# Kernel optimization log

Measured on AMD Instinct MI355X. Metric: run time of the kernel, lower is better.

The kernel has to match this reference:

```python
import jax, jax.numpy as jnp
import numpy as np

PARENTS = [-1, 0, 0, 0, 1, 2, 3, 4, 5, 6, 7, 8, 9, 9, 9, 12, 13, 14, 16, 17, 18, 19, 20, 21]
K = 24          # num_joints (SMPL kinematic tree)
BONE = 12       # 3x3 rotation (9) + 3 rel offset
FEAT = 64       # local_feature_size
B = 65536       # batch
NIN = BONE + 1 + FEAT  # 77: bone_transform(13) concat parent feature(64)


def setup_inputs() -> dict:
    key = jax.random.key(0)
    ks = jax.random.split(key, 6)
    pose = jax.random.normal(ks[0], (B, K, 3, 3), jnp.float32)
    rel_joints = jax.random.normal(ks[1], (B, K, 3), jnp.float32)
    # proj_bone_prior: Linear(K*BONE -> FEAT)
    Wp = jax.random.normal(ks[2], (K * BONE, FEAT), jnp.float32) * 0.05
    bp = jnp.zeros((FEAT,), jnp.float32)
    # per-joint BoneMLP: Linear(NIN->NIN), ReLU, Linear(NIN->FEAT), ReLU (stacked over K)
    W1 = jax.random.normal(ks[3], (K, NIN, NIN), jnp.float32) * 0.05
    b1 = jnp.zeros((K, NIN), jnp.float32)
    W2 = jax.random.normal(ks[4], (K, NIN, FEAT), jnp.float32) * 0.05
    b2 = jnp.zeros((K, FEAT), jnp.float32)
    return {"pose": pose, "rel_joints": rel_joints, "Wp": Wp, "bp": bp,
            "W1": W1, "b1": b1, "W2": W2, "b2": b2}


def reference(pose, rel_joints, Wp, bp, W1, b1, W2, b2):
    Bn, Kn = rel_joints.shape[0], rel_joints.shape[1]
    bone_lengths = jnp.linalg.norm(rel_joints, axis=-1, keepdims=True)          # B,K,1
    bone_features = jnp.concatenate([pose.reshape(Bn, Kn, 9), rel_joints], -1)  # B,K,12
    root_bone_prior = bone_features.reshape(Bn, -1) @ Wp + bp                   # B,FEAT
    bone_transforms = jnp.concatenate([bone_features, bone_lengths], -1)        # B,K,13
    feats = [None] * Kn
    for i in range(Kn):  # fixed structural loop over kinematic tree (K=24)
        parent = PARENTS[i]
        pf = root_bone_prior if parent == -1 else feats[parent]
        x = jnp.concatenate([bone_transforms[:, i, :], pf], axis=-1)  # B,77
        h = jax.nn.relu(x @ W1[i] + b1[i])
        feats[i] = jax.nn.relu(h @ W2[i] + b2[i])
    return jnp.concatenate(feats, axis=-1)  # B, K*FEAT
```

## Files before the change

### kernel.cpp

```cpp
#include <hip/hip_runtime.h>
#include <hip/hip_bf16.h>
#include <math.h>

typedef __attribute__((ext_vector_type(8))) short short8;
typedef __attribute__((ext_vector_type(4))) short s4;
typedef __attribute__((ext_vector_type(4))) float f32x4;

#define NJ 24

#define F1_J   7680
#define F2_OFF (NJ*F1_J)
#define F2_J   6144
#define FP_OFF (F2_OFF + NJ*F2_J)
#define IMG_SHORTS (FP_OFF + 36*512)

#define MFMA(A,B,C) __builtin_amdgcn_mfma_f32_16x16x32_bf16((A),(B),(C),0,0,0)

__constant__ int ORD[24] = {0,1,4,7,10, 2,5,8,11, 3,6,9, 12,15, 13,16,18,20,22, 14,17,19,21,23};
__constant__ int PSL[24] = {2,0,1,1,1,  0,1,1,1,  0,0,0,  0,1,   0,1,1,1,1,    0,0,0,0,0};
__constant__ int SSL[24] = {0,1,1,1,-1, 1,1,1,-1, 0,0,0,  1,-1,  1,1,1,1,-1,   0,0,0,0,-1};

__device__ __forceinline__ short f2bf(float f) {
  union { float f; unsigned u; } v; v.f = f;
  unsigned r = v.u + 0x7FFFu + ((v.u >> 16) & 1u);
  return (short)(r >> 16);
}
__device__ __forceinline__ short sbf(float f) {
  __hip_bfloat16 h = __float2bfloat16(f);
  return *reinterpret_cast<short*>(&h);
}
__device__ __forceinline__ short8 pk8(f32x4 lo, f32x4 hi) {
  union { short8 s; unsigned u[4]; } r;
  asm("v_cvt_pk_bf16_f32 %0, %1, %2" : "=v"(r.u[0]) : "v"(lo[0]), "v"(lo[1]));
  asm("v_cvt_pk_bf16_f32 %0, %1, %2" : "=v"(r.u[1]) : "v"(lo[2]), "v"(lo[3]));
  asm("v_cvt_pk_bf16_f32 %0, %1, %2" : "=v"(r.u[2]) : "v"(hi[0]), "v"(hi[1]));
  asm("v_cvt_pk_bf16_f32 %0, %1, %2" : "=v"(r.u[3]) : "v"(hi[2]), "v"(hi[3]));
  return r.s;
}
__device__ __forceinline__ s4 pk4(f32x4 v) {
  union { s4 s; unsigned u[2]; } r;
  asm("v_cvt_pk_bf16_f32 %0, %1, %2" : "=v"(r.u[0]) : "v"(v[0]), "v"(v[1]));
  asm("v_cvt_pk_bf16_f32 %0, %1, %2" : "=v"(r.u[1]) : "v"(v[2]), "v"(v[3]));
  return r.s;
}
__device__ __forceinline__ f32x4 relu4(f32x4 v) {
  f32x4 r; r[0]=fmaxf(v[0],0.f); r[1]=fmaxf(v[1],0.f);
  r[2]=fmaxf(v[2],0.f); r[3]=fmaxf(v[3],0.f); return r;
}

__global__ __launch_bounds__(256) void prep_kernel(
    const float* __restrict__ W1, const float* __restrict__ W2,
    const float* __restrict__ Wp, const float* __restrict__ b1,
    const float* __restrict__ b2, short* __restrict__ img) {
  int t = blockIdx.x * 256 + threadIdx.x;
  if (t >= IMG_SHORTS) return;
  float v = 0.f;
  if (t < F2_OFF) {
    int i = t / F1_J, r = t % F1_J;
    int blk = r >> 9, q = r & 511;
    int ln = q >> 3, e = q & 7;
    int nt = blk / 3, s = blk - nt*3;
    int n  = nt*16 + (ln & 15);
    int kp = s*32 + (ln >> 4)*8 + e;
    if (kp == 13) {
      v = (n < 77) ? b1[i*77 + n] : (n == 77 ? 1.f : 0.f);
    } else if (n < 77) {
      if (kp < 13)                  v = W1[i*5929 + kp*77 + n];
      else if (kp >= 16 && kp < 80) v = W1[i*5929 + (kp-3)*77 + n];
    }
  } else if (t < FP_OFF) {
    int u = t - F2_OFF;
    int i = u / F2_J, r = u % F2_J;
    int blk = r >> 9, q = r & 511;
    int ln = q >> 3, e = q & 7;
    int nt = blk / 3, s = blk - nt*3;
    int n  = nt*16 + (ln & 15);
    int k  = s*32 + (ln >> 4)*8 + e;
    if (k < 77)       v = W2[i*4928 + k*64 + n];
    else if (k == 77) v = b2[i*64 + n];
  } else {
    int u = t - FP_OFF;
    int blk = u >> 9, q = u & 511;
    int ln = q >> 3, e = q & 7;
    int nt = blk / 9, s = blk - nt*9;
    int n  = nt*16 + (ln & 15);
    int kp = s*32 + (ln >> 4)*8 + e;
    int j, w;
    if (kp < 216) { j = kp / 9;       w = kp % 9; }
    else          { j = (kp-216) / 3; w = 9 + (kp-216) % 3; }
    v = Wp[(j*12 + w)*64 + n];
  }
  img[t] = f2bf(v);
}

#define ISSUE_W1(JN) do { \
  unsigned long long _b = img_u + (unsigned long long)(JN)*15360ull; \
  asm volatile( \
    "global_load_dwordx4 %0, %15, %16\n"  "global_load_dwordx4 %1, %15, %16 offset:1024\n" \
    "global_load_dwordx4 %2, %15, %16 offset:2048\n" "global_load_dwordx4 %3, %15, %16 offset:3072\n" \
    "global_load_dwordx4 %4, %15, %17\n"  "global_load_dwordx4 %5, %15, %17 offset:1024\n" \
    "global_load_dwordx4 %6, %15, %17 offset:2048\n" "global_load_dwordx4 %7, %15, %17 offset:3072\n" \
    "global_load_dwordx4 %8, %15, %18\n"  "global_load_dwordx4 %9, %15, %18 offset:1024\n" \
    "global_load_dwordx4 %10, %15, %18 offset:2048\n" "global_load_dwordx4 %11, %15, %18 offset:3072\n" \
    "global_load_dwordx4 %12, %15, %19\n" "global_load_dwordx4 %13, %15, %19 offset:1024\n" \
    "global_load_dwordx4 %14, %15, %19 offset:2048\n" \
    : "=&v"(fw1[0]),"=&v"(fw1[1]),"=&v"(fw1[2]),"=&v"(fw1[3]),"=&v"(fw1[4]), \
      "=&v"(fw1[5]),"=&v"(fw1[6]),"=&v"(fw1[7]),"=&v"(fw1[8]),"=&v"(fw1[9]), \
      "=&v"(fw1[10]),"=&v"(fw1[11]),"=&v"(fw1[12]),"=&v"(fw1[13]),"=&v"(fw1[14]) \
    : "v"(voff), "s"(_b), "s"(_b+4096ull), "s"(_b+8192ull), "s"(_b+12288ull) \
    : "memory"); \
} while(0)

#define ISSUE_BTW2(J) do { \
  unsigned long long _b = img_u + 368640ull + (unsigned long long)(J)*12288ull; \
  asm volatile( \
    "global_load_dword %0, %20, off\n" \
    "global_load_dword %1, %20, off offset:4\n" \
    "global_load_dword %2, %20, off offset:8\n" \
    "global_load_dword %3, %20, off offset:12\n" \
    "global_load_dword %4, %21, %22\n" \
    "global_load_dword %5, %21, %22 offset:4\n" \
    "global_load_dword %6, %21, %22 offset:8\n" \
    "global_load_dword %7, %21, %22 offset:12\n" \
    "global_load_dwordx4 %8, %23, %24\n"  "global_load_dwordx4 %9, %23, %24 offset:1024\n" \
    "global_load_dwordx4 %10, %23, %24 offset:2048\n" "global_load_dwordx4 %11, %23, %24 offset:3072\n" \
    "global_load_dwordx4 %12, %23, %25\n" "global_load_dwordx4 %13, %23, %25 offset:1024\n" \
    "global_load_dwordx4 %14, %23, %25 offset:2048\n" "global_load_dwordx4 %15, %23, %25 offset:3072\n" \
    "global_load_dwordx4 %16, %23, %26\n" "global_load_dwordx4 %17, %23, %26 offset:1024\n" \
    "global_load_dwordx4 %18, %23, %26 offset:2048\n" "global_load_dwordx4 %19, %23, %26 offset:3072\n" \
    : "=&v"(d0),"=&v"(d1),"=&v"(d2),"=&v"(d3),"=&v"(d4),"=&v"(d5),"=&v"(d6),"=&v"(d7), \
      "=&v"(fw2[0]),"=&v"(fw2[1]),"=&v"(fw2[2]),"=&v"(fw2[3]),"=&v"(fw2[4]),"=&v"(fw2[5]), \
      "=&v"(fw2[6]),"=&v"(fw2[7]),"=&v"(fw2[8]),"=&v"(fw2[9]),"=&v"(fw2[10]),"=&v"(fw2[11]) \
    : "v"(aA), "v"(vB), "s"(pose_u), "v"(voff), \
      "s"(_b), "s"(_b+4096ull), "s"(_b+8192ull) \
    : "memory"); \
} while(0)

#define WAITV(N) do { asm volatile("s_waitcnt vmcnt(" #N ")" ::: "memory"); \
                      __builtin_amdgcn_sched_barrier(0); } while(0)

__global__ __launch_bounds__(256, 2) void enc_kernel(
    const float* __restrict__ pose, const float* __restrict__ rel,
    const float* __restrict__ bp,  const short* __restrict__ img,
    float* __restrict__ out) {
  __shared__ __align__(16) short lds[4*10240];

  const int tid  = threadIdx.x;
  const int lane = tid & 63;
  const int wv   = tid >> 6;
  short* myl   = lds + wv*10240;
  short* featL = myl;
  short* hL    = myl + 6912;
  short* btL   = myl + 9472;

  const int cl  = lane & 15;
  const int g   = lane >> 4;
  const int rw0 = blockIdx.x*128 + wv*32;
  const short8 zz = {0,0,0,0,0,0,0,0};
  const unsigned long long img_u  = (unsigned long long)img;
  const unsigned long long pose_u = (unsigned long long)pose;
  const unsigned long long rel_u  = (unsigned long long)rel;
  const unsigned voff = (unsigned)lane << 4;
  const int btr = lane >> 1, btq = lane & 1;
  const unsigned btProw = (unsigned)((rw0 + btr)*864);
  const unsigned btRrow = (unsigned)((rw0 + btr)*288);

  short8 fw1[15], fw2[12];
  float d0, d1, d2, d3, d4, d5, d6, d7;

  {
    const float* pb = pose + (size_t)(rw0 + btr)*216;
    const float* rb = rel  + (size_t)(rw0 + btr)*72;
    short8 w;
    if (btq == 0) {
      w = pk8(*(const f32x4*)pb, *(const f32x4*)(pb + 4));
    } else {
      float r0 = rb[0], r1 = rb[1], r2 = rb[2];
      float nv = sqrtf(r0*r0 + r1*r1 + r2*r2);
      w[0]=sbf(pb[8]); w[1]=sbf(r0); w[2]=sbf(r1); w[3]=sbf(r2);
      w[4]=sbf(nv); w[5]=(short)0x3F80; w[6]=0; w[7]=0;
    }
    *(short8*)(btL + btr*24 + btq*8) = w;
  }
  f32x4 bpv[4];
#pragma unroll
  for (int nt = 0; nt < 4; ++nt) bpv[nt] = *(const f32x4*)(bp + nt*16 + g*4);

  f32x4 racc[2][4] = {};
  {
    const float* pr0 = pose + (size_t)(rw0 + cl)*216;
    const float* rr0 = rel  + (size_t)(rw0 + cl)*72;
    const float* pr1 = pose + (size_t)(rw0 + 16 + cl)*216;
    const float* rr1 = rel  + (size_t)(rw0 + 16 + cl)*72;
    const short8* fpg = (const short8*)(img + FP_OFF) + lane;
    short8 av0[9], av1[9];
#pragma unroll
    for (int s = 0; s < 9; ++s) {
      int k0 = s*32 + g*8;
      const float* s0 = (k0 < 216) ? (pr0 + k0) : (rr0 + (k0 - 216));
      const float* s1 = (k0 < 216) ? (pr1 + k0) : (rr1 + (k0 - 216));
      av0[s] = pk8(*(const f32x4*)s0, *(const f32x4*)(s0 + 4));
      av1[s] = pk8(*(const f32x4*)s1, *(const f32x4*)(s1 + 4));
    }
#pragma unroll
    for (int nt = 0; nt < 4; ++nt) {
      short8 fwp[9];
#pragma unroll
      for (int s = 0; s < 9; ++s) fwp[s] = fpg[(nt*9 + s)*64];
#pragma unroll
      for (int s = 0; s < 9; ++s) {
        racc[0][nt] = MFMA(fwp[s], av0[s], racc[0][nt]);
        racc[1][nt] = MFMA(fwp[s], av1[s], racc[1][nt]);
      }
    }
  }
#pragma unroll
  for (int nt = 0; nt < 4; ++nt) {
#pragma unroll
    for (int m = 0; m < 2; ++m) {
      f32x4 v = racc[m][nt];
      v[0]+=bpv[nt][0]; v[1]+=bpv[nt][1]; v[2]+=bpv[nt][2]; v[3]+=bpv[nt][3];
      *(s4*)(featL + 2*2304 + (m*16 + cl)*72 + nt*16 + g*4) = pk4(v);
    }
  }

  ISSUE_W1(0);

#pragma unroll 1
  for (int p = 0; p < NJ; ++p) {
    const int j  = ORD[p];
    const int ps = PSL[p];
    const int ss = SSL[p];
    const int jn = (p < NJ-1) ? ORD[p+1] : 0;

    const short* fb0 = featL + ps*2304 + cl*72;
    const short* fb1 = featL + ps*2304 + (16 + cl)*72;
    short8 a0[2], a1[2], a2[2];
    a0[0] = (g < 2) ? *(const short8*)(btL + cl*24 + g*8)
                    : *(const short8*)(fb0 + (g-2)*8);
    a0[1] = (g < 2) ? *(const short8*)(btL + (16+cl)*24 + g*8)
                    : *(const short8*)(fb1 + (g-2)*8);
    a1[0] = *(const short8*)(fb0 + 16 + g*8);
    a1[1] = *(const short8*)(fb1 + 16 + g*8);
    a2[0] = (g < 2) ? *(const short8*)(fb0 + 48 + g*8) : zz;
    a2[1] = (g < 2) ? *(const short8*)(fb1 + 48 + g*8) : zz;

    const unsigned long long aA =
        btq ? (rel_u  + btRrow + (unsigned)(jn ? jn*12 - 4 : 0))
            : (pose_u + btProw + (unsigned)(jn*36));
    const unsigned vB = btProw + (unsigned)(jn*36) + (btq ? 20u : 16u);
    ISSUE_BTW2(j);

    if (p == 0) { WAITV(20); } else { WAITV(28); }

#pragma unroll
    for (int nt = 0; nt < 5; ++nt) {
      f32x4 c0 = {0,0,0,0}, c1 = {0,0,0,0};
      c0 = MFMA(fw1[nt*3+0], a0[0], c0);  c1 = MFMA(fw1[nt*3+0], a0[1], c1);
      c0 = MFMA(fw1[nt*3+1], a1[0], c0);  c1 = MFMA(fw1[nt*3+1], a1[1], c1);
      c0 = MFMA(fw1[nt*3+2], a2[0], c0);  c1 = MFMA(fw1[nt*3+2], a2[1], c1);
      *(s4*)(hL + cl*80 + nt*16 + g*4)        = pk4(relu4(c0));
      *(s4*)(hL + (16 + cl)*80 + nt*16 + g*4) = pk4(relu4(c1));
    }
    short8 h0[2], h1[2], h2[2];
#pragma unroll
    for (int m = 0; m < 2; ++m) {
      const short* hb = hL + (m*16 + cl)*80;
      h0[m] = *(const short8*)(hb + g*8);
      h1[m] = *(const short8*)(hb + 32 + g*8);
      h2[m] = (g < 2) ? *(const short8*)(hb + 64 + g*8) : zz;
    }

    ISSUE_W1(jn);
    WAITV(15);

    {
      f32x4 lo = {d0, d1, d2, d3}, hi = {d4, d5, d6, d7};
      short8 wA = pk8(lo, hi);
      float r0 = jn ? d1 : d0;
      float r1 = jn ? d2 : d1;
      float r2 = jn ? d3 : d2;
      float nv = sqrtf(r0*r0 + r1*r1 + r2*r2);
      short8 wB;
      wB[0]=sbf(d7);   wB[1]=sbf(r0); wB[2]=sbf(r1); wB[3]=sbf(r2);
      wB[4]=sbf(nv); wB[5]=(short)0x3F80; wB[6]=0; wB[7]=0;
      short8 w = btq ? wB : wA;
      *(short8*)(btL + btr*24 + btq*8) = w;
    }

#pragma unroll
    for (int nt = 0; nt < 4; ++nt) {
      f32x4 c0 = {0,0,0,0}, c1 = {0,0,0,0};
      c0 = MFMA(fw2[nt*3+0], h0[0], c0);  c1 = MFMA(fw2[nt*3+0], h0[1], c1);
      c0 = MFMA(fw2[nt*3+1], h1[0], c0);  c1 = MFMA(fw2[nt*3+1], h1[1], c1);
      c0 = MFMA(fw2[nt*3+2], h2[0], c0);  c1 = MFMA(fw2[nt*3+2], h2[1], c1);
      f32x4 v0 = relu4(c0), v1 = relu4(c1);
      float* o0 = out + (size_t)(rw0 + cl)*1536      + (size_t)j*64 + nt*16 + g*4;
      float* o1 = out + (size_t)(rw0 + 16 + cl)*1536 + (size_t)j*64 + nt*16 + g*4;
      __builtin_nontemporal_store(v0, (f32x4*)o0);
      __builtin_nontemporal_store(v1, (f32x4*)o1);
      if (ss >= 0) {
        *(s4*)(featL + ss*2304 + cl*72 + nt*16 + g*4)        = pk4(v0);
        *(s4*)(featL + ss*2304 + (16 + cl)*72 + nt*16 + g*4) = pk4(v1);
      }
    }
  }
}

extern "C" void kernel_launch(void* const* d_in, const int* in_sizes, int n_in,
                              void* d_out, int out_size, void* d_ws, size_t ws_size,
                              hipStream_t stream) {
  const float* pose = (const float*)d_in[0];
  const float* rel  = (const float*)d_in[1];
  const float* Wp   = (const float*)d_in[2];
  const float* bp   = (const float*)d_in[3];
  const float* W1   = (const float*)d_in[4];
  const float* b1   = (const float*)d_in[5];
  const float* W2   = (const float*)d_in[6];
  const float* b2   = (const float*)d_in[7];
  float* outp = (float*)d_out;
  short* img  = (short*)d_ws;
  const int Bn = in_sizes[0] / 216;
  prep_kernel<<<(IMG_SHORTS + 255)/256, 256, 0, stream>>>(W1, W2, Wp, b1, b2, img);
  enc_kernel<<<Bn/128, 256, 0, stream>>>(pose, rel, bp, img, outp);
}
```

Measured before the change: 153.4 us.

## Double-buffer W1 fragments and prefetch weights two joints ahead

Splits the W1 register fragments into two alternating buffers so W1 for joint p+2 is loaded while joint p computes, and moves the W2/bone-transform loads to the end of each iteration so they prefetch one joint ahead. The loop is unrolled by two to alternate buffers, the wait counts are re-tuned, and the W2 loads are reordered ahead of the dword loads. The bone-transform LDS row stride also shrinks from 24 to 16. This lengthens the load-to-use distance to hide global latency, at the cost of 15 more short8 registers per thread, which may hurt occupancy or spill under launch_bounds(256,2).

```diff
diff --git a/kernel.cpp b/kernel.cpp
--- a/kernel.cpp
+++ b/kernel.cpp
@@ -93,7 +93,7 @@
   img[t] = f2bf(v);
 }
 
-#define ISSUE_W1(JN) do { \
+#define ISSUE_W1_INTO(ARR, JN) do { \
   unsigned long long _b = img_u + (unsigned long long)(JN)*15360ull; \
   asm volatile( \
     "global_load_dwordx4 %0, %15, %16\n"  "global_load_dwordx4 %1, %15, %16 offset:1024\n" \
@@ -104,9 +104,9 @@
     "global_load_dwordx4 %10, %15, %18 offset:2048\n" "global_load_dwordx4 %11, %15, %18 offset:3072\n" \
     "global_load_dwordx4 %12, %15, %19\n" "global_load_dwordx4 %13, %15, %19 offset:1024\n" \
     "global_load_dwordx4 %14, %15, %19 offset:2048\n" \
-    : "=&v"(fw1[0]),"=&v"(fw1[1]),"=&v"(fw1[2]),"=&v"(fw1[3]),"=&v"(fw1[4]), \
-      "=&v"(fw1[5]),"=&v"(fw1[6]),"=&v"(fw1[7]),"=&v"(fw1[8]),"=&v"(fw1[9]), \
-      "=&v"(fw1[10]),"=&v"(fw1[11]),"=&v"(fw1[12]),"=&v"(fw1[13]),"=&v"(fw1[14]) \
+    : "=&v"(ARR[0]),"=&v"(ARR[1]),"=&v"(ARR[2]),"=&v"(ARR[3]),"=&v"(ARR[4]), \
+      "=&v"(ARR[5]),"=&v"(ARR[6]),"=&v"(ARR[7]),"=&v"(ARR[8]),"=&v"(ARR[9]), \
+      "=&v"(ARR[10]),"=&v"(ARR[11]),"=&v"(ARR[12]),"=&v"(ARR[13]),"=&v"(ARR[14]) \
     : "v"(voff), "s"(_b), "s"(_b+4096ull), "s"(_b+8192ull), "s"(_b+12288ull) \
     : "memory"); \
 } while(0)
@@ -114,6 +114,12 @@
 #define ISSUE_BTW2(J) do { \
   unsigned long long _b = img_u + 368640ull + (unsigned long long)(J)*12288ull; \
   asm volatile( \
+    "global_load_dwordx4 %8, %23, %24\n"  "global_load_dwordx4 %9, %23, %24 offset:1024\n" \
+    "global_load_dwordx4 %10, %23, %24 offset:2048\n" "global_load_dwordx4 %11, %23, %24 offset:3072\n" \
+    "global_load_dwordx4 %12, %23, %25\n" "global_load_dwordx4 %13, %23, %25 offset:1024\n" \
+    "global_load_dwordx4 %14, %23, %25 offset:2048\n" "global_load_dwordx4 %15, %23, %25 offset:3072\n" \
+    "global_load_dwordx4 %16, %23, %26\n" "global_load_dwordx4 %17, %23, %26 offset:1024\n" \
+    "global_load_dwordx4 %18, %23, %26 offset:2048\n" "global_load_dwordx4 %19, %23, %26 offset:3072\n" \
     "global_load_dword %0, %20, off\n" \
     "global_load_dword %1, %20, off offset:4\n" \
     "global_load_dword %2, %20, off offset:8\n" \
@@ -122,12 +128,6 @@
     "global_load_dword %5, %21, %22 offset:4\n" \
     "global_load_dword %6, %21, %22 offset:8\n" \
     "global_load_dword %7, %21, %22 offset:12\n" \
-    "global_load_dwordx4 %8, %23, %24\n"  "global_load_dwordx4 %9, %23, %24 offset:1024\n" \
-    "global_load_dwordx4 %10, %23, %24 offset:2048\n" "global_load_dwordx4 %11, %23, %24 offset:3072\n" \
-    "global_load_dwordx4 %12, %23, %25\n" "global_load_dwordx4 %13, %23, %25 offset:1024\n" \
-    "global_load_dwordx4 %14, %23, %25 offset:2048\n" "global_load_dwordx4 %15, %23, %25 offset:3072\n" \
-    "global_load_dwordx4 %16, %23, %26\n" "global_load_dwordx4 %17, %23, %26 offset:1024\n" \
-    "global_load_dwordx4 %18, %23, %26 offset:2048\n" "global_load_dwordx4 %19, %23, %26 offset:3072\n" \
     : "=&v"(d0),"=&v"(d1),"=&v"(d2),"=&v"(d3),"=&v"(d4),"=&v"(d5),"=&v"(d6),"=&v"(d7), \
       "=&v"(fw2[0]),"=&v"(fw2[1]),"=&v"(fw2[2]),"=&v"(fw2[3]),"=&v"(fw2[4]),"=&v"(fw2[5]), \
       "=&v"(fw2[6]),"=&v"(fw2[7]),"=&v"(fw2[8]),"=&v"(fw2[9]),"=&v"(fw2[10]),"=&v"(fw2[11]) \
@@ -138,6 +138,91 @@
 
 #define WAITV(N) do { asm volatile("s_waitcnt vmcnt(" #N ")" ::: "memory"); \
                       __builtin_amdgcn_sched_barrier(0); } while(0)
+
+#define BODY(P, FW, CWAIT) do { \
+    const int j  = ORD[P]; \
+    const int ps = PSL[P]; \
+    const int ss = SSL[P]; \
+    const int jw2 = ((P)+1 < NJ) ? ORD[(P)+1] : 0; \
+    const int jd  = ((P)+1 < NJ) ? ORD[(P)+1] : 0; \
+    const int jb  = ((P)+2 < NJ) ? ORD[(P)+2] : 0; \
+    const int jw1 = ((P)+2 < NJ) ? ORD[(P)+2] : 0; \
+     \
+    const short* fb0 = featL + ps*2304 + cl*72; \
+    const short* fb1 = featL + ps*2304 + (16 + cl)*72; \
+    short8 a0[2], a1[2], a2[2]; \
+    a0[0] = (g < 2) ? *(const short8*)(btL + cl*16 + g*8) \
+                    : *(const short8*)(fb0 + (g-2)*8); \
+    a0[1] = (g < 2) ? *(const short8*)(btL + (16+cl)*16 + g*8) \
+                    : *(const short8*)(fb1 + (g-2)*8); \
+    a1[0] = *(const short8*)(fb0 + 16 + g*8); \
+    a1[1] = *(const short8*)(fb1 + 16 + g*8); \
+    a2[0] = (g < 2) ? *(const short8*)(fb0 + 48 + g*8) : zz; \
+    a2[1] = (g < 2) ? *(const short8*)(fb1 + 48 + g*8) : zz; \
+     \
+    WAITV(CWAIT); \
+     \
+    _Pragma("unroll") \
+    for (int nt = 0; nt < 5; ++nt) { \
+      f32x4 c0 = {0,0,0,0}, c1 = {0,0,0,0}; \
+      c0 = MFMA(FW[nt*3+0], a0[0], c0);  c1 = MFMA(FW[nt*3+0], a0[1], c1); \
+      c0 = MFMA(FW[nt*3+1], a1[0], c0);  c1 = MFMA(FW[nt*3+1], a1[1], c1); \
+      c0 = MFMA(FW[nt*3+2], a2[0], c0);  c1 = MFMA(FW[nt*3+2], a2[1], c1); \
+      *(s4*)(hL + cl*80 + nt*16 + g*4)        = pk4(relu4(c0)); \
+      *(s4*)(hL + (16 + cl)*80 + nt*16 + g*4) = pk4(relu4(c1)); \
+    } \
+     \
+    short8 h0[2], h1[2], h2[2]; \
+    _Pragma("unroll") \
+    for (int m = 0; m < 2; ++m) { \
+      const short* hb = hL + (m*16 + cl)*80; \
+      h0[m] = *(const short8*)(hb + g*8); \
+      h1[m] = *(const short8*)(hb + 32 + g*8); \
+      h2[m] = (g < 2) ? *(const short8*)(hb + 64 + g*8) : zz; \
+    } \
+     \
+    WAITV(15); \
+     \
+    { \
+      f32x4 lo = {d0, d1, d2, d3}, hi = {d4, d5, d6, d7}; \
+      short8 wA = pk8(lo, hi); \
+      float r0 = jd ? d1 : d0; \
+      float r1 = jd ? d2 : d1; \
+      float r2 = jd ? d3 : d2; \
+      float nv = sqrtf(r0*r0 + r1*r1 + r2*r2); \
+      short8 wB; \
+      wB[0]=sbf(d7);   wB[1]=sbf(r0); wB[2]=sbf(r1); wB[3]=sbf(r2); \
+      wB[4]=sbf(nv); wB[5]=(short)0x3F80; wB[6]=0; wB[7]=0; \
+      short8 w = btq ? wB : wA; \
+      *(short8*)(btL + btr*16 + btq*8) = w; \
+    } \
+     \
+    _Pragma("unroll") \
+    for (int nt = 0; nt < 4; ++nt) { \
+      f32x4 c0 = {0,0,0,0}, c1 = {0,0,0,0}; \
+      c0 = MFMA(fw2[nt*3+0], h0[0], c0);  c1 = MFMA(fw2[nt*3+0], h0[1], c1); \
+      c0 = MFMA(fw2[nt*3+1], h1[0], c0);  c1 = MFMA(fw2[nt*3+1], h1[1], c1); \
+      c0 = MFMA(fw2[nt*3+2], h2[0], c0);  c1 = MFMA(fw2[nt*3+2], h2[1], c1); \
+      f32x4 v0 = relu4(c0), v1 = relu4(c1); \
+      float* o0 = out + (size_t)(rw0 + cl)*1536      + (size_t)j*64 + nt*16 + g*4; \
+      float* o1 = out + (size_t)(rw0 + 16 + cl)*1536 + (size_t)j*64 + nt*16 + g*4; \
+      __builtin_nontemporal_store(v0, (f32x4*)o0); \
+      __builtin_nontemporal_store(v1, (f32x4*)o1); \
+      if (ss >= 0) { \
+        *(s4*)(featL + ss*2304 + cl*72 + nt*16 + g*4)        = pk4(v0); \
+        *(s4*)(featL + ss*2304 + (16 + cl)*72 + nt*16 + g*4) = pk4(v1); \
+      } \
+    } \
+     \
+    { \
+      const unsigned long long aA = \
+          btq ? (rel_u  + btRrow + (unsigned)(jb ? jb*12 - 4 : 0)) \
+              : (pose_u + btProw + (unsigned)(jb*36)); \
+      const unsigned vB = btProw + (unsigned)(jb*36) + (btq ? 20u : 16u); \
+      ISSUE_BTW2(jw2); \
+    } \
+    ISSUE_W1_INTO(FW, jw1); \
+  } while(0)
 
 __global__ __launch_bounds__(256, 2) void enc_kernel(
     const float* __restrict__ pose, const float* __restrict__ rel,
@@ -165,7 +250,7 @@
   const unsigned btProw = (unsigned)((rw0 + btr)*864);
   const unsigned btRrow = (unsigned)((rw0 + btr)*288);
 
-  short8 fw1[15], fw2[12];
+  short8 fw1a[15], fw1b[15], fw2[12];
   float d0, d1, d2, d3, d4, d5, d6, d7;
 
   {
@@ -180,7 +265,7 @@
       w[0]=sbf(pb[8]); w[1]=sbf(r0); w[2]=sbf(r1); w[3]=sbf(r2);
       w[4]=sbf(nv); w[5]=(short)0x3F80; w[6]=0; w[7]=0;
     }
-    *(short8*)(btL + btr*24 + btq*8) = w;
+    *(short8*)(btL + btr*16 + btq*8) = w;
   }
   f32x4 bpv[4];
 #pragma unroll
@@ -224,86 +309,24 @@
     }
   }
 
-  ISSUE_W1(0);
-
+  {
+    const int jb = ORD[1];
+    const unsigned long long aA =
+        btq ? (rel_u  + btRrow + (unsigned)(jb*12 - 4))
+            : (pose_u + btProw + (unsigned)(jb*36));
+    const unsigned vB = btProw + (unsigned)(jb*36) + (btq ? 20u : 16u);
+    ISSUE_BTW2(0);
+  }
+  ISSUE_W1_INTO(fw1a, 0);
+  ISSUE_W1_INTO(fw1b, ORD[1]);
+
+  BODY(0, fw1a, 15);
+  BODY(1, fw1b, 43);
 #pragma unroll 1
-  for (int p = 0; p < NJ; ++p) {
-    const int j  = ORD[p];
-    const int ps = PSL[p];
-    const int ss = SSL[p];
-    const int jn = (p < NJ-1) ? ORD[p+1] : 0;
-
-    const short* fb0 = featL + ps*2304 + cl*72;
-    const short* fb1 = featL + ps*2304 + (16 + cl)*72;
-    short8 a0[2], a1[2], a2[2];
-    a0[0] = (g < 2) ? *(const short8*)(btL + cl*24 + g*8)
-                    : *(const short8*)(fb0 + (g-2)*8);
-    a0[1] = (g < 2) ? *(const short8*)(btL + (16+cl)*24 + g*8)
-                    : *(const short8*)(fb1 + (g-2)*8);
-    a1[0] = *(const short8*)(fb0 + 16 + g*8);
-    a1[1] = *(const short8*)(fb1 + 16 + g*8);
-    a2[0] = (g < 2) ? *(const short8*)(fb0 + 48 + g*8) : zz;
-    a2[1] = (g < 2) ? *(const short8*)(fb1 + 48 + g*8) : zz;
-
-    const unsigned long long aA =
-        btq ? (rel_u  + btRrow + (unsigned)(jn ? jn*12 - 4 : 0))
-            : (pose_u + btProw + (unsigned)(jn*36));
-    const unsigned vB = btProw + (unsigned)(jn*36) + (btq ? 20u : 16u);
-    ISSUE_BTW2(j);
-
-    if (p == 0) { WAITV(20); } else { WAITV(28); }
-
-#pragma unroll
-    for (int nt = 0; nt < 5; ++nt) {
-      f32x4 c0 = {0,0,0,0}, c1 = {0,0,0,0};
-      c0 = MFMA(fw1[nt*3+0], a0[0], c0);  c1 = MFMA(fw1[nt*3+0], a0[1], c1);
-      c0 = MFMA(fw1[nt*3+1], a1[0], c0);  c1 = MFMA(fw1[nt*3+1], a1[1], c1);
-      c0 = MFMA(fw1[nt*3+2], a2[0], c0);  c1 = MFMA(fw1[nt*3+2], a2[1], c1);
-      *(s4*)(hL + cl*80 + nt*16 + g*4)        = pk4(relu4(c0));
-      *(s4*)(hL + (16 + cl)*80 + nt*16 + g*4) = pk4(relu4(c1));
-    }
-    short8 h0[2], h1[2], h2[2];
-#pragma unroll
-    for (int m = 0; m < 2; ++m) {
-      const short* hb = hL + (m*16 + cl)*80;
-      h0[m] = *(const short8*)(hb + g*8);
-      h1[m] = *(const short8*)(hb + 32 + g*8);
-      h2[m] = (g < 2) ? *(const short8*)(hb + 64 + g*8) : zz;
-    }
-
-    ISSUE_W1(jn);
-    WAITV(15);
-
-    {
-      f32x4 lo = {d0, d1, d2, d3}, hi = {d4, d5, d6, d7};
-      short8 wA = pk8(lo, hi);
-      float r0 = jn ? d1 : d0;
-      float r1 = jn ? d2 : d1;
-      float r2 = jn ? d3 : d2;
-      float nv = sqrtf(r0*r0 + r1*r1 + r2*r2);
-      short8 wB;
-      wB[0]=sbf(d7);   wB[1]=sbf(r0); wB[2]=sbf(r1); wB[3]=sbf(r2);
-      wB[4]=sbf(nv); wB[5]=(short)0x3F80; wB[6]=0; wB[7]=0;
-      short8 w = btq ? wB : wA;
-      *(short8*)(btL + btr*24 + btq*8) = w;
-    }
-
-#pragma unroll
-    for (int nt = 0; nt < 4; ++nt) {
-      f32x4 c0 = {0,0,0,0}, c1 = {0,0,0,0};
-      c0 = MFMA(fw2[nt*3+0], h0[0], c0);  c1 = MFMA(fw2[nt*3+0], h0[1], c1);
-      c0 = MFMA(fw2[nt*3+1], h1[0], c0);  c1 = MFMA(fw2[nt*3+1], h1[1], c1);
-      c0 = MFMA(fw2[nt*3+2], h2[0], c0);  c1 = MFMA(fw2[nt*3+2], h2[1], c1);
-      f32x4 v0 = relu4(c0), v1 = relu4(c1);
-      float* o0 = out + (size_t)(rw0 + cl)*1536      + (size_t)j*64 + nt*16 + g*4;
-      float* o1 = out + (size_t)(rw0 + 16 + cl)*1536 + (size_t)j*64 + nt*16 + g*4;
-      __builtin_nontemporal_store(v0, (f32x4*)o0);
-      __builtin_nontemporal_store(v1, (f32x4*)o1);
-      if (ss >= 0) {
-        *(s4*)(featL + ss*2304 + cl*72 + nt*16 + g*4)        = pk4(v0);
-        *(s4*)(featL + ss*2304 + (16 + cl)*72 + nt*16 + g*4) = pk4(v1);
-      }
-    }
+  for (int q = 1; q < 12; ++q) {
+    const int p = 2*q;
+    BODY(p,     fw1a, 43);
+    BODY(p + 1, fw1b, 43);
   }
 }
 
```

Result: no change. 152.9 us (-0.4%).

## Process 64 rows per wave to halve weight reloads per row

Applied to the files above, without the earlier changes.

Each wave now covers 64 batch rows instead of 32, so the per-joint W1/W2 fragments loaded into registers are reused across four 16-row MFMA tiles. The grid is halved, LDS per wave grows, and launch bounds drop to one block per CU. Bone-transform loading is simplified to one lane per row with scalar dword loads, and the load/wait schedule is reordered. The aim is to cut weight traffic per row, at the cost of less parallelism for hiding latency and a full vmcnt(0) wait on each joint.

```diff
diff --git a/kernel.cpp b/kernel.cpp
--- a/kernel.cpp
+++ b/kernel.cpp
@@ -17,7 +17,7 @@
 #define MFMA(A,B,C) __builtin_amdgcn_mfma_f32_16x16x32_bf16((A),(B),(C),0,0,0)
 
 __constant__ int ORD[24] = {0,1,4,7,10, 2,5,8,11, 3,6,9, 12,15, 13,16,18,20,22, 14,17,19,21,23};
-__constant__ int PSL[24] = {2,0,1,1,1,  0,1,1,1,  0,0,0,  0,1,   0,1,1,1,1,    0,0,0,0,0};
+__constant__ int PSL[24] = {1,0,1,1,1,  0,1,1,1,  0,0,0,  0,1,   0,1,1,1,1,    0,0,0,0,0};
 __constant__ int SSL[24] = {0,1,1,1,-1, 1,1,1,-1, 0,0,0,  1,-1,  1,1,1,1,-1,   0,0,0,0,-1};
 
 __device__ __forceinline__ short f2bf(float f) {
@@ -114,24 +114,29 @@
 #define ISSUE_BTW2(J) do { \
   unsigned long long _b = img_u + 368640ull + (unsigned long long)(J)*12288ull; \
   asm volatile( \
-    "global_load_dword %0, %20, off\n" \
-    "global_load_dword %1, %20, off offset:4\n" \
-    "global_load_dword %2, %20, off offset:8\n" \
-    "global_load_dword %3, %20, off offset:12\n" \
-    "global_load_dword %4, %21, %22\n" \
-    "global_load_dword %5, %21, %22 offset:4\n" \
-    "global_load_dword %6, %21, %22 offset:8\n" \
-    "global_load_dword %7, %21, %22 offset:12\n" \
-    "global_load_dwordx4 %8, %23, %24\n"  "global_load_dwordx4 %9, %23, %24 offset:1024\n" \
-    "global_load_dwordx4 %10, %23, %24 offset:2048\n" "global_load_dwordx4 %11, %23, %24 offset:3072\n" \
-    "global_load_dwordx4 %12, %23, %25\n" "global_load_dwordx4 %13, %23, %25 offset:1024\n" \
-    "global_load_dwordx4 %14, %23, %25 offset:2048\n" "global_load_dwordx4 %15, %23, %25 offset:3072\n" \
-    "global_load_dwordx4 %16, %23, %26\n" "global_load_dwordx4 %17, %23, %26 offset:1024\n" \
-    "global_load_dwordx4 %18, %23, %26 offset:2048\n" "global_load_dwordx4 %19, %23, %26 offset:3072\n" \
-    : "=&v"(d0),"=&v"(d1),"=&v"(d2),"=&v"(d3),"=&v"(d4),"=&v"(d5),"=&v"(d6),"=&v"(d7), \
+    "global_load_dwordx4 %12, %26, %27\n" "global_load_dwordx4 %13, %26, %27 offset:1024\n" \
+    "global_load_dwordx4 %14, %26, %27 offset:2048\n" "global_load_dwordx4 %15, %26, %27 offset:3072\n" \
+    "global_load_dwordx4 %16, %26, %28\n" "global_load_dwordx4 %17, %26, %28 offset:1024\n" \
+    "global_load_dwordx4 %18, %26, %28 offset:2048\n" "global_load_dwordx4 %19, %26, %28 offset:3072\n" \
+    "global_load_dwordx4 %20, %26, %29\n" "global_load_dwordx4 %21, %26, %29 offset:1024\n" \
+    "global_load_dwordx4 %22, %26, %29 offset:2048\n" "global_load_dwordx4 %23, %26, %29 offset:3072\n" \
+    "global_load_dword %0, %24, off\n" \
+    "global_load_dword %1, %24, off offset:4\n" \
+    "global_load_dword %2, %24, off offset:8\n" \
+    "global_load_dword %3, %24, off offset:12\n" \
+    "global_load_dword %4, %24, off offset:16\n" \
+    "global_load_dword %5, %24, off offset:20\n" \
+    "global_load_dword %6, %24, off offset:24\n" \
+    "global_load_dword %7, %24, off offset:28\n" \
+    "global_load_dword %8, %24, off offset:32\n" \
+    "global_load_dword %9, %25, off\n" \
+    "global_load_dword %10, %25, off offset:4\n" \
+    "global_load_dword %11, %25, off offset:8\n" \
+    : "=&v"(d0),"=&v"(d1),"=&v"(d2),"=&v"(d3),"=&v"(d4),"=&v"(d5), \
+      "=&v"(d6),"=&v"(d7),"=&v"(d8),"=&v"(d9),"=&v"(d10),"=&v"(d11), \
       "=&v"(fw2[0]),"=&v"(fw2[1]),"=&v"(fw2[2]),"=&v"(fw2[3]),"=&v"(fw2[4]),"=&v"(fw2[5]), \
       "=&v"(fw2[6]),"=&v"(fw2[7]),"=&v"(fw2[8]),"=&v"(fw2[9]),"=&v"(fw2[10]),"=&v"(fw2[11]) \
-    : "v"(aA), "v"(vB), "s"(pose_u), "v"(voff), \
+    : "v"(aP), "v"(aR), "v"(voff), \
       "s"(_b), "s"(_b+4096ull), "s"(_b+8192ull) \
     : "memory"); \
 } while(0)
@@ -139,88 +144,68 @@
 #define WAITV(N) do { asm volatile("s_waitcnt vmcnt(" #N ")" ::: "memory"); \
                       __builtin_amdgcn_sched_barrier(0); } while(0)
 
-__global__ __launch_bounds__(256, 2) void enc_kernel(
+__global__ __launch_bounds__(256, 1) void enc_kernel(
     const float* __restrict__ pose, const float* __restrict__ rel,
     const float* __restrict__ bp,  const short* __restrict__ img,
     float* __restrict__ out) {
-  __shared__ __align__(16) short lds[4*10240];
+  __shared__ __align__(16) short lds[4*15360];
 
   const int tid  = threadIdx.x;
   const int lane = tid & 63;
   const int wv   = tid >> 6;
-  short* myl   = lds + wv*10240;
+  short* myl   = lds + wv*15360;
   short* featL = myl;
-  short* hL    = myl + 6912;
-  short* btL   = myl + 9472;
+  short* hL    = myl + 9216;
+  short* btL   = myl + 14336;
 
   const int cl  = lane & 15;
   const int g   = lane >> 4;
-  const int rw0 = blockIdx.x*128 + wv*32;
+  const int rw0 = blockIdx.x*256 + wv*64;
   const short8 zz = {0,0,0,0,0,0,0,0};
   const unsigned long long img_u  = (unsigned long long)img;
   const unsigned long long pose_u = (unsigned long long)pose;
   const unsigned long long rel_u  = (unsigned long long)rel;
   const unsigned voff = (unsigned)lane << 4;
-  const int btr = lane >> 1, btq = lane & 1;
-  const unsigned btProw = (unsigned)((rw0 + btr)*864);
-  const unsigned btRrow = (unsigned)((rw0 + btr)*288);
+  const unsigned long long btP = pose_u + (unsigned long long)(rw0 + lane)*864ull;
+  const unsigned long long btR = rel_u  + (unsigned long long)(rw0 + lane)*288ull;
 
   short8 fw1[15], fw2[12];
-  float d0, d1, d2, d3, d4, d5, d6, d7;
+  float d0,d1,d2,d3,d4,d5,d6,d7,d8,d9,d10,d11;
 
   {
-    const float* pb = pose + (size_t)(rw0 + btr)*216;
-    const float* rb = rel  + (size_t)(rw0 + btr)*72;
-    short8 w;
-    if (btq == 0) {
-      w = pk8(*(const f32x4*)pb, *(const f32x4*)(pb + 4));
-    } else {
-      float r0 = rb[0], r1 = rb[1], r2 = rb[2];
-      float nv = sqrtf(r0*r0 + r1*r1 + r2*r2);
-      w[0]=sbf(pb[8]); w[1]=sbf(r0); w[2]=sbf(r1); w[3]=sbf(r2);
-      w[4]=sbf(nv); w[5]=(short)0x3F80; w[6]=0; w[7]=0;
-    }
-    *(short8*)(btL + btr*24 + btq*8) = w;
-  }
-  f32x4 bpv[4];
-#pragma unroll
-  for (int nt = 0; nt < 4; ++nt) bpv[nt] = *(const f32x4*)(bp + nt*16 + g*4);
-
-  f32x4 racc[2][4] = {};
-  {
-    const float* pr0 = pose + (size_t)(rw0 + cl)*216;
-    const float* rr0 = rel  + (size_t)(rw0 + cl)*72;
-    const float* pr1 = pose + (size_t)(rw0 + 16 + cl)*216;
-    const float* rr1 = rel  + (size_t)(rw0 + 16 + cl)*72;
+    const float* pb = pose + (size_t)(rw0 + lane)*216;
+    const float* rb = rel  + (size_t)(rw0 + lane)*72;
+    float p0=pb[0],p1=pb[1],p2=pb[2],p3=pb[3],p4=pb[4],p5=pb[5],p6=pb[6],p7=pb[7],p8=pb[8];
+    float r0=rb[0],r1=rb[1],r2=rb[2];
+    float nv = sqrtf(r0*r0 + r1*r1 + r2*r2);
+    short8 wlo = pk8((f32x4){p0,p1,p2,p3}, (f32x4){p4,p5,p6,p7});
+    short8 whi;
+    whi[0]=sbf(p8); whi[1]=sbf(r0); whi[2]=sbf(r1); whi[3]=sbf(r2);
+    whi[4]=sbf(nv); whi[5]=(short)0x3F80; whi[6]=0; whi[7]=0;
+    *(short8*)(btL + lane*16)     = wlo;
+    *(short8*)(btL + lane*16 + 8) = whi;
+  }
+
+#pragma unroll 1
+  for (int m = 0; m < 4; ++m) {
+    const float* pr = pose + (size_t)(rw0 + m*16 + cl)*216;
+    const float* rr = rel  + (size_t)(rw0 + m*16 + cl)*72;
     const short8* fpg = (const short8*)(img + FP_OFF) + lane;
-    short8 av0[9], av1[9];
+    short8 av[9];
 #pragma unroll
     for (int s = 0; s < 9; ++s) {
       int k0 = s*32 + g*8;
-      const float* s0 = (k0 < 216) ? (pr0 + k0) : (rr0 + (k0 - 216));
-      const float* s1 = (k0 < 216) ? (pr1 + k0) : (rr1 + (k0 - 216));
-      av0[s] = pk8(*(const f32x4*)s0, *(const f32x4*)(s0 + 4));
-      av1[s] = pk8(*(const f32x4*)s1, *(const f32x4*)(s1 + 4));
+      const float* sp = (k0 < 216) ? (pr + k0) : (rr + (k0 - 216));
+      av[s] = pk8(*(const f32x4*)sp, *(const f32x4*)(sp + 4));
     }
 #pragma unroll
     for (int nt = 0; nt < 4; ++nt) {
-      short8 fwp[9];
-#pragma unroll
-      for (int s = 0; s < 9; ++s) fwp[s] = fpg[(nt*9 + s)*64];
-#pragma unroll
-      for (int s = 0; s < 9; ++s) {
-        racc[0][nt] = MFMA(fwp[s], av0[s], racc[0][nt]);
-        racc[1][nt] = MFMA(fwp[s], av1[s], racc[1][nt]);
-      }
-    }
-  }
-#pragma unroll
-  for (int nt = 0; nt < 4; ++nt) {
-#pragma unroll
-    for (int m = 0; m < 2; ++m) {
-      f32x4 v = racc[m][nt];
-      v[0]+=bpv[nt][0]; v[1]+=bpv[nt][1]; v[2]+=bpv[nt][2]; v[3]+=bpv[nt][3];
-      *(s4*)(featL + 2*2304 + (m*16 + cl)*72 + nt*16 + g*4) = pk4(v);
+      f32x4 c = {0,0,0,0};
+#pragma unroll
+      for (int s = 0; s < 9; ++s) c = MFMA(fpg[(nt*9 + s)*64], av[s], c);
+      f32x4 bb = *(const f32x4*)(bp + nt*16 + g*4);
+      c[0]+=bb[0]; c[1]+=bb[1]; c[2]+=bb[2]; c[3]+=bb[3];
+      *(s4*)(featL + 4608 + (m*16 + cl)*72 + nt*16 + g*4) = pk4(c);
     }
   }
 
@@ -233,77 +218,62 @@
     const int ss = SSL[p];
     const int jn = (p < NJ-1) ? ORD[p+1] : 0;
 
-    const short* fb0 = featL + ps*2304 + cl*72;
-    const short* fb1 = featL + ps*2304 + (16 + cl)*72;
-    short8 a0[2], a1[2], a2[2];
-    a0[0] = (g < 2) ? *(const short8*)(btL + cl*24 + g*8)
-                    : *(const short8*)(fb0 + (g-2)*8);
-    a0[1] = (g < 2) ? *(const short8*)(btL + (16+cl)*24 + g*8)
-                    : *(const short8*)(fb1 + (g-2)*8);
-    a1[0] = *(const short8*)(fb0 + 16 + g*8);
-    a1[1] = *(const short8*)(fb1 + 16 + g*8);
-    a2[0] = (g < 2) ? *(const short8*)(fb0 + 48 + g*8) : zz;
-    a2[1] = (g < 2) ? *(const short8*)(fb1 + 48 + g*8) : zz;
-
-    const unsigned long long aA =
-        btq ? (rel_u  + btRrow + (unsigned)(jn ? jn*12 - 4 : 0))
-            : (pose_u + btProw + (unsigned)(jn*36));
-    const unsigned vB = btProw + (unsigned)(jn*36) + (btq ? 20u : 16u);
+    const unsigned long long aP = btP + (unsigned long long)(jn*36);
+    const unsigned long long aR = btR + (unsigned long long)(jn*12);
     ISSUE_BTW2(j);
 
-    if (p == 0) { WAITV(20); } else { WAITV(28); }
-
-#pragma unroll
-    for (int nt = 0; nt < 5; ++nt) {
-      f32x4 c0 = {0,0,0,0}, c1 = {0,0,0,0};
-      c0 = MFMA(fw1[nt*3+0], a0[0], c0);  c1 = MFMA(fw1[nt*3+0], a0[1], c1);
-      c0 = MFMA(fw1[nt*3+1], a1[0], c0);  c1 = MFMA(fw1[nt*3+1], a1[1], c1);
-      c0 = MFMA(fw1[nt*3+2], a2[0], c0);  c1 = MFMA(fw1[nt*3+2], a2[1], c1);
-      *(s4*)(hL + cl*80 + nt*16 + g*4)        = pk4(relu4(c0));
-      *(s4*)(hL + (16 + cl)*80 + nt*16 + g*4) = pk4(relu4(c1));
-    }
-    short8 h0[2], h1[2], h2[2];
-#pragma unroll
-    for (int m = 0; m < 2; ++m) {
+    WAITV(24);
+
+#pragma unroll
+    for (int m = 0; m < 4; ++m) {
+      const short* fb = featL + ps*4608 + (m*16 + cl)*72;
+      short8 a0 = (g < 2) ? *(const short8*)(btL + (m*16 + cl)*16 + g*8)
+                          : *(const short8*)(fb + (g-2)*8);
+      short8 a1 = *(const short8*)(fb + 16 + g*8);
+      short8 a2 = (g < 2) ? *(const short8*)(fb + 48 + g*8) : zz;
+#pragma unroll
+      for (int nt = 0; nt < 5; ++nt) {
+        f32x4 c = {0,0,0,0};
+        c = MFMA(fw1[nt*3+0], a0, c);
+        c = MFMA(fw1[nt*3+1], a1, c);
+        c = MFMA(fw1[nt*3+2], a2, c);
+        *(s4*)(hL + (m*16 + cl)*80 + nt*16 + g*4) = pk4(relu4(c));
+      }
+    }
+
+    WAITV(0);
+
+    {
+      float nv = sqrtf(d9*d9 + d10*d10 + d11*d11);
+      short8 wlo = pk8((f32x4){d0,d1,d2,d3}, (f32x4){d4,d5,d6,d7});
+      short8 whi;
+      whi[0]=sbf(d8); whi[1]=sbf(d9); whi[2]=sbf(d10); whi[3]=sbf(d11);
+      whi[4]=sbf(nv); whi[5]=(short)0x3F80; whi[6]=0; whi[7]=0;
+      *(short8*)(btL + lane*16)     = wlo;
+      *(short8*)(btL + lane*16 + 8) = whi;
+    }
+
+#pragma unroll
+    for (int m = 0; m < 4; ++m) {
       const short* hb = hL + (m*16 + cl)*80;
-      h0[m] = *(const short8*)(hb + g*8);
-      h1[m] = *(const short8*)(hb + 32 + g*8);
-      h2[m] = (g < 2) ? *(const short8*)(hb + 64 + g*8) : zz;
+      short8 h0 = *(const short8*)(hb + g*8);
+      short8 h1 = *(const short8*)(hb + 32 + g*8);
+      short8 h2 = (g < 2) ? *(const short8*)(hb + 64 + g*8) : zz;
+#pragma unroll
+      for (int nt = 0; nt < 4; ++nt) {
+        f32x4 c = {0,0,0,0};
+        c = MFMA(fw2[nt*3+0], h0, c);
+        c = MFMA(fw2[nt*3+1], h1, c);
+        c = MFMA(fw2[nt*3+2], h2, c);
+        f32x4 v = relu4(c);
+        float* o = out + (size_t)(rw0 + m*16 + cl)*1536 + (size_t)j*64 + nt*16 + g*4;
+        __builtin_nontemporal_store(v, (f32x4*)o);
+        if (ss >= 0)
+          *(s4*)(featL + ss*4608 + (m*16 + cl)*72 + nt*16 + g*4) = pk4(v);
+      }
     }
 
     ISSUE_W1(jn);
-    WAITV(15);
-
-    {
-      f32x4 lo = {d0, d1, d2, d3}, hi = {d4, d5, d6, d7};
-      short8 wA = pk8(lo, hi);
-      float r0 = jn ? d1 : d0;
-      float r1 = jn ? d2 : d1;
-      float r2 = jn ? d3 : d2;
-      float nv = sqrtf(r0*r0 + r1*r1 + r2*r2);
-      short8 wB;
-      wB[0]=sbf(d7);   wB[1]=sbf(r0); wB[2]=sbf(r1); wB[3]=sbf(r2);
-      wB[4]=sbf(nv); wB[5]=(short)0x3F80; wB[6]=0; wB[7]=0;
-      short8 w = btq ? wB : wA;
-      *(short8*)(btL + btr*24 + btq*8) = w;
-    }
-
-#pragma unroll
-    for (int nt = 0; nt < 4; ++nt) {
-      f32x4 c0 = {0,0,0,0}, c1 = {0,0,0,0};
-      c0 = MFMA(fw2[nt*3+0], h0[0], c0);  c1 = MFMA(fw2[nt*3+0], h0[1], c1);
-      c0 = MFMA(fw2[nt*3+1], h1[0], c0);  c1 = MFMA(fw2[nt*3+1], h1[1], c1);
-      c0 = MFMA(fw2[nt*3+2], h2[0], c0);  c1 = MFMA(fw2[nt*3+2], h2[1], c1);
-      f32x4 v0 = relu4(c0), v1 = relu4(c1);
-      float* o0 = out + (size_t)(rw0 + cl)*1536      + (size_t)j*64 + nt*16 + g*4;
-      float* o1 = out + (size_t)(rw0 + 16 + cl)*1536 + (size_t)j*64 + nt*16 + g*4;
-      __builtin_nontemporal_store(v0, (f32x4*)o0);
-      __builtin_nontemporal_store(v1, (f32x4*)o1);
-      if (ss >= 0) {
-        *(s4*)(featL + ss*2304 + cl*72 + nt*16 + g*4)        = pk4(v0);
-        *(s4*)(featL + ss*2304 + (16 + cl)*72 + nt*16 + g*4) = pk4(v1);
-      }
-    }
   }
 }
 
@@ -322,5 +292,5 @@
   short* img  = (short*)d_ws;
   const int Bn = in_sizes[0] / 216;
   prep_kernel<<<(IMG_SHORTS + 255)/256, 256, 0, stream>>>(W1, W2, Wp, b1, b2, img);
-  enc_kernel<<<Bn/128, 256, 0, stream>>>(pose, rel, bp, img, outp);
-}
+  enc_kernel<<<Bn/256, 256, 0, stream>>>(pose, rel, bp, img, outp);
+}
```

New measurement: 149.0 us. -2.9%, faster.
